# Kernel optimization log

Measured on AMD Instinct MI355X. Metric: run time of the kernel, lower is better.

## Reference

```python
import jax, jax.numpy as jnp
from jax import lax
import numpy as np

N_BITS = 108
N_OUT = 7
# pos_bits[i, j] = bit j (MSB-first) of index i, matching `i >> (6 - j) & 1`
POS_BITS = np.array([[(i >> (6 - j)) & 1 for j in range(N_OUT)] for i in range(N_BITS)], dtype=np.float32)
# LZC value when all 108 bits are zero: 108 = 1101100b, MSB first
LZC_108 = np.array([1, 1, 0, 1, 1, 0, 0], dtype=np.float32)


def setup_inputs() -> dict:
    key = jax.random.key(0)
    # sparse binary bits so leading-zero runs are long and some rows are all-zero
    X = (jax.random.uniform(key, (2_000_000, N_BITS)) < 0.03).astype(jnp.float32)
    return {"X": X}


def _lzd(X):
    """X: [..., 108] MSB-first bits -> [..., 7] LZC MSB-first.

    Arithmetic soft-gate semantics: NOT(a)=1-a, AND(a,b)=a*b,
    OR(a,b)=a+b-a*b, MUX(s,a,b)=s*a+(1-s)*b, OR-tree = 1-prod(1-x).
    Sequential carry over `found` expressed with lax.scan (108 steps).
    """
    batch_shape = X.shape[:-1]
    bits = jnp.moveaxis(X, -1, 0)  # [108, ...]
    pos = jnp.asarray(POS_BITS, dtype=X.dtype)  # [108, 7]

    def step(carry, inp):
        found, lzc = carry                  # found: [..., 1], lzc: [..., 7]
        bit, pos_bits = inp                 # bit: [...], pos_bits: [7]
        bit = bit[..., None]                # [..., 1]
        not_found = 1.0 - found             # NOT
        is_first = bit * not_found          # AND
        # MUX per output bit: is_first ? pos_bit : lzc
        lzc = is_first * pos_bits + (1.0 - is_first) * lzc
        # OR: found | is_first
        found = found + is_first - found * is_first
        return (found, lzc), None

    found0 = jnp.zeros(batch_shape + (1,), X.dtype)
    lzc0 = jnp.zeros(batch_shape + (N_OUT,), X.dtype)
    (found, lzc), _ = lax.scan(step, (found0, lzc0), (bits, pos))

    # OR-tree over all 108 bits, then all-zero override with LZC=108
    any_one = 1.0 - jnp.prod(1.0 - X, axis=-1, keepdims=True)  # [..., 1]
    all_zero = 1.0 - any_one                                   # NOT
    lzc108 = jnp.asarray(LZC_108, dtype=X.dtype)               # [7]
    return all_zero * lzc108 + (1.0 - all_zero) * lzc


def reference(X):
    return _lzd(X)
```

## Files before the change

kernel.cpp:

```cpp
#include <hip/hip_runtime.h>


#define LZD_NBITS 108
#define LZD_NOUT 7
#define RPB 256
#define F4R 27
#define F4B (RPB * F4R)
#define KPAD 28

static __device__ __forceinline__ unsigned umin_(unsigned a, unsigned b) {
    return a < b ? a : b;
}

__global__ __launch_bounds__(256) void lzd108_kernel(const float* __restrict__ X,
                                                     float* __restrict__ out,
                                                     int n_rows) {
    __shared__ unsigned short keys[RPB][KPAD];
    const int tid = threadIdx.x;
    const size_t row0 = (size_t)blockIdx.x * RPB;
    const float4* __restrict__ p =
        reinterpret_cast<const float4*>(X) + row0 * F4R;

    keys[tid][F4R] = (unsigned short)0xFFFFu;

    const size_t nf4_rem = ((size_t)n_rows - row0) * F4R;

    if (nf4_rem >= (size_t)F4B) {
        #pragma unroll
        for (int it = 0; it < F4B / RPB; ++it) {
            const int i = tid + it * RPB;
            const float4 v = p[i];
            const int r = i / F4R;
            const int c = i - r * F4R;
            const unsigned sub = (v.x != 0.0f) ? 0u
                               : (v.y != 0.0f) ? 1u
                               : (v.z != 0.0f) ? 2u
                               : (v.w != 0.0f) ? 3u : 4u;
            keys[r][c] = (sub == 4u) ? (unsigned short)0xFFFFu
                                     : (unsigned short)(4u * (unsigned)c + sub);
        }
    } else {
        const int nf4 = (int)nf4_rem;
        #pragma unroll 1
        for (int i = tid; i < nf4; i += RPB) {
            const float4 v = p[i];
            const int r = i / F4R;
            const int c = i - r * F4R;
            const unsigned sub = (v.x != 0.0f) ? 0u
                               : (v.y != 0.0f) ? 1u
                               : (v.z != 0.0f) ? 2u
                               : (v.w != 0.0f) ? 3u : 4u;
            keys[r][c] = (sub == 4u) ? (unsigned short)0xFFFFu
                                     : (unsigned short)(4u * (unsigned)c + sub);
        }
    }
    __syncthreads();

    const size_t row = row0 + (size_t)tid;
    if (row < (size_t)n_rows) {
        const uint2* kp = reinterpret_cast<const uint2*>(&keys[tid][0]);
        unsigned m = 0xFFFFu;
        #pragma unroll
        for (int j = 0; j < 7; ++j) {
            const uint2 u = kp[j];
            m = umin_(m, umin_(umin_(u.x & 0xFFFFu, u.x >> 16),
                               umin_(u.y & 0xFFFFu, u.y >> 16)));
        }
        const unsigned idx = (m > 107u) ? (unsigned)LZD_NBITS : m;
        float* o = out + row * LZD_NOUT;
        o[0] = (float)((idx >> 6) & 1u);
        o[1] = (float)((idx >> 5) & 1u);
        o[2] = (float)((idx >> 4) & 1u);
        o[3] = (float)((idx >> 3) & 1u);
        o[4] = (float)((idx >> 2) & 1u);
        o[5] = (float)((idx >> 1) & 1u);
        o[6] = (float)(idx & 1u);
    }
}

extern "C" void kernel_launch(void* const* d_in, const int* in_sizes, int n_in,
                              void* d_out, int out_size, void* d_ws, size_t ws_size,
                              hipStream_t stream) {
    const float* X = (const float*)d_in[0];
    float* out = (float*)d_out;
    int n_rows = in_sizes[0] / LZD_NBITS;
    int block = 256;
    int grid = (n_rows + RPB - 1) / RPB;
    lzd108_kernel<<<grid, block, 0, stream>>>(X, out, n_rows);
}
```

Before: 1.116 ms.

## Stage outputs in shared memory for coalesced stores and batch loads in groups

Per-thread output writes, which were strided by 7 floats, are replaced by staging the results in shared memory and then issuing coalesced block-wide stores. Input loads are issued in groups of 9 per iteration instead of a fully unrolled loop, which bounds register pressure while keeping several loads in flight. The zero test now uses integer comparisons instead of float comparisons. The cost is an extra barrier and more shared memory. Integer tests would treat -0.0 as nonzero, which cannot occur with these binary inputs.

```diff
diff --git a/kernel.cpp b/kernel.cpp
--- a/kernel.cpp
+++ b/kernel.cpp
@@ -2,79 +2,98 @@
 
 
 #define LZD_NBITS 108
-#define LZD_NOUT 7
-#define RPB 256
-#define F4R 27
-#define F4B (RPB * F4R)
+#define LZD_NOUT  7
+#define RPB  256
+#define F4R  27
+#define F4B  (RPB * F4R)
 #define KPAD 28
-
-static __device__ __forceinline__ unsigned umin_(unsigned a, unsigned b) {
-    return a < b ? a : b;
-}
+#define GRP  9
 
 __global__ __launch_bounds__(256) void lzd108_kernel(const float* __restrict__ X,
                                                      float* __restrict__ out,
                                                      int n_rows) {
     __shared__ unsigned short keys[RPB][KPAD];
+    __shared__ float outs[RPB * LZD_NOUT];
+
     const int tid = threadIdx.x;
     const size_t row0 = (size_t)blockIdx.x * RPB;
-    const float4* __restrict__ p =
-        reinterpret_cast<const float4*>(X) + row0 * F4R;
+    const uint4* __restrict__ p =
+        reinterpret_cast<const uint4*>(X) + row0 * F4R;
 
     keys[tid][F4R] = (unsigned short)0xFFFFu;
 
     const size_t nf4_rem = ((size_t)n_rows - row0) * F4R;
 
     if (nf4_rem >= (size_t)F4B) {
-        #pragma unroll
-        for (int it = 0; it < F4B / RPB; ++it) {
-            const int i = tid + it * RPB;
-            const float4 v = p[i];
-            const int r = i / F4R;
-            const int c = i - r * F4R;
-            const unsigned sub = (v.x != 0.0f) ? 0u
-                               : (v.y != 0.0f) ? 1u
-                               : (v.z != 0.0f) ? 2u
-                               : (v.w != 0.0f) ? 3u : 4u;
-            keys[r][c] = (sub == 4u) ? (unsigned short)0xFFFFu
-                                     : (unsigned short)(4u * (unsigned)c + sub);
+        #pragma unroll 1
+        for (int g = 0; g < F4R / GRP; ++g) {
+            uint4 v[GRP];
+            #pragma unroll
+            for (int u = 0; u < GRP; ++u)
+                v[u] = p[tid + (g * GRP + u) * RPB];
+            #pragma unroll
+            for (int u = 0; u < GRP; ++u) {
+                const int i = tid + (g * GRP + u) * RPB;
+                const int r = i / F4R;
+                const int c = i - r * F4R;
+                const uint4 w = v[u];
+                const unsigned sub = w.x ? 0u : w.y ? 1u : w.z ? 2u
+                                   : w.w ? 3u : 4u;
+                keys[r][c] = (sub == 4u)
+                                 ? (unsigned short)0xFFFFu
+                                 : (unsigned short)(4u * (unsigned)c + sub);
+            }
         }
     } else {
         const int nf4 = (int)nf4_rem;
         #pragma unroll 1
         for (int i = tid; i < nf4; i += RPB) {
-            const float4 v = p[i];
+            const uint4 w = p[i];
             const int r = i / F4R;
             const int c = i - r * F4R;
-            const unsigned sub = (v.x != 0.0f) ? 0u
-                               : (v.y != 0.0f) ? 1u
-                               : (v.z != 0.0f) ? 2u
-                               : (v.w != 0.0f) ? 3u : 4u;
-            keys[r][c] = (sub == 4u) ? (unsigned short)0xFFFFu
-                                     : (unsigned short)(4u * (unsigned)c + sub);
+            const unsigned sub = w.x ? 0u : w.y ? 1u : w.z ? 2u
+                               : w.w ? 3u : 4u;
+            keys[r][c] = (sub == 4u)
+                             ? (unsigned short)0xFFFFu
+                             : (unsigned short)(4u * (unsigned)c + sub);
         }
     }
     __syncthreads();
 
-    const size_t row = row0 + (size_t)tid;
-    if (row < (size_t)n_rows) {
+    const int nvalid_l = n_rows - (int)row0;
+    const int nvalid = nvalid_l < RPB ? nvalid_l : RPB;
+
+    if (tid < nvalid) {
         const uint2* kp = reinterpret_cast<const uint2*>(&keys[tid][0]);
         unsigned m = 0xFFFFu;
         #pragma unroll
         for (int j = 0; j < 7; ++j) {
             const uint2 u = kp[j];
-            m = umin_(m, umin_(umin_(u.x & 0xFFFFu, u.x >> 16),
-                               umin_(u.y & 0xFFFFu, u.y >> 16)));
+            const unsigned a = u.x & 0xFFFFu, b = u.x >> 16;
+            const unsigned c2 = u.y & 0xFFFFu, d = u.y >> 16;
+            const unsigned ab = a < b ? a : b;
+            const unsigned cd = c2 < d ? c2 : d;
+            const unsigned e = ab < cd ? ab : cd;
+            m = m < e ? m : e;
         }
         const unsigned idx = (m > 107u) ? (unsigned)LZD_NBITS : m;
-        float* o = out + row * LZD_NOUT;
-        o[0] = (float)((idx >> 6) & 1u);
-        o[1] = (float)((idx >> 5) & 1u);
-        o[2] = (float)((idx >> 4) & 1u);
-        o[3] = (float)((idx >> 3) & 1u);
-        o[4] = (float)((idx >> 2) & 1u);
-        o[5] = (float)((idx >> 1) & 1u);
-        o[6] = (float)(idx & 1u);
+        float* os = &outs[tid * LZD_NOUT];
+        os[0] = (float)((idx >> 6) & 1u);
+        os[1] = (float)((idx >> 5) & 1u);
+        os[2] = (float)((idx >> 4) & 1u);
+        os[3] = (float)((idx >> 3) & 1u);
+        os[4] = (float)((idx >> 2) & 1u);
+        os[5] = (float)((idx >> 1) & 1u);
+        os[6] = (float)(idx & 1u);
+    }
+    __syncthreads();
+
+    const int limit = nvalid * LZD_NOUT;
+    float* ob = out + row0 * LZD_NOUT;
+    #pragma unroll
+    for (int j = 0; j < LZD_NOUT; ++j) {
+        const int k = tid + j * RPB;
+        if (k < limit) ob[k] = outs[k];
     }
 }
 
```

Result: faster. 1.088 ms (-2.5%).

## Early-exit per-row scan with bitmask ffs, two rows per thread

Applied to the files above, without the earlier changes.

Replaces the coalesced full-row load plus shared-memory min reduction with a per-thread scan that handles two rows. Each thread loads 16-float chunks, packs their sign/exponent bits into a mask, and stops at the first nonzero chunk, so it can skip reading the rest of the row. Outputs for the two rows are written together as float2 stores. The cost is uncoalesced, divergent per-thread loads, which may lower effective bandwidth. With 3% density, most rows find a set bit within the first one or two chunks, though whole cache lines are still fetched.

```diff
diff --git a/kernel.cpp b/kernel.cpp
--- a/kernel.cpp
+++ b/kernel.cpp
@@ -3,78 +3,93 @@
 
 #define LZD_NBITS 108
 #define LZD_NOUT 7
-#define RPB 256
-#define F4R 27
-#define F4B (RPB * F4R)
-#define KPAD 28
 
-static __device__ __forceinline__ unsigned umin_(unsigned a, unsigned b) {
-    return a < b ? a : b;
-}
+#define MASK16(a, b, c, d)                                              \
+    ( ((a).x >> 23 & 1u)   | ((a).y >> 22 & 2u)   |                     \
+      ((a).z >> 21 & 4u)   | ((a).w >> 20 & 8u)   |                     \
+      ((b).x >> 19 & 16u)  | ((b).y >> 18 & 32u)  |                     \
+      ((b).z >> 17 & 64u)  | ((b).w >> 16 & 128u) |                     \
+      ((c).x >> 15 & 256u) | ((c).y >> 14 & 512u) |                     \
+      ((c).z >> 13 & 1024u)| ((c).w >> 12 & 2048u)|                     \
+      ((d).x >> 11 & 4096u)| ((d).y >> 10 & 8192u)|                     \
+      ((d).z >> 9 & 16384u)| ((d).w >> 8 & 32768u) )
+
+#define ROW_ROUND(P, off, etot, pos, done)                              \
+    if (!(done)) {                                                      \
+        const int e_ = (etot) - 16 * k;                                 \
+        if (k < 7 || e_ > 0) {                                          \
+            uint4 a_, b_, c_, d_;                                       \
+            a_ = (P)[4 * k];                                            \
+            if (k < 6) {                                                \
+                b_ = (P)[4 * k + 1];                                    \
+                c_ = (P)[4 * k + 2];                                    \
+                d_ = (P)[4 * k + 3];                                    \
+            } else if (k == 6) {                                        \
+                b_ = (P)[4 * k + 1];                                    \
+                c_ = (P)[4 * k + 2];                                    \
+                d_ = make_uint4(0u, 0u, 0u, 0u);                        \
+                if (e_ > 12) d_ = (P)[4 * k + 3];                       \
+            } else {                                                    \
+                b_ = make_uint4(0u, 0u, 0u, 0u);                        \
+                c_ = make_uint4(0u, 0u, 0u, 0u);                        \
+                d_ = make_uint4(0u, 0u, 0u, 0u);                        \
+                if (e_ > 4) b_ = (P)[4 * k + 1];                        \
+            }                                                           \
+            unsigned m_ = MASK16(a_, b_, c_, d_);                       \
+            if (k == 0) m_ &= ~((1u << (off)) - 1u);                    \
+            if (k >= 6) { if (e_ < 16) m_ &= (1u << e_) - 1u; }         \
+            if (m_) {                                                   \
+                (pos) = 16 * k + (__ffs(m_) - 1) - (int)(off);          \
+                (done) = true;                                          \
+            } else if (k >= 6 && e_ <= 16) {                            \
+                (done) = true;            \
+            }                                                           \
+        } else {                                                        \
+            (done) = true;                                              \
+        }                                                               \
+    }
 
 __global__ __launch_bounds__(256) void lzd108_kernel(const float* __restrict__ X,
                                                      float* __restrict__ out,
                                                      int n_rows) {
-    __shared__ unsigned short keys[RPB][KPAD];
-    const int tid = threadIdx.x;
-    const size_t row0 = (size_t)blockIdx.x * RPB;
-    const float4* __restrict__ p =
-        reinterpret_cast<const float4*>(X) + row0 * F4R;
+    const int t = blockIdx.x * blockDim.x + threadIdx.x;
+    const int r0 = 2 * t;
+    if (r0 >= n_rows) return;
+    const bool has1 = (r0 + 1) < n_rows;
 
-    keys[tid][F4R] = (unsigned short)0xFFFFu;
+    const unsigned off0 = (unsigned)(((unsigned)r0 * 108u) & 15u);
+    const unsigned off1 = (unsigned)(((unsigned)(r0 + 1) * 108u) & 15u);
+    const uint4* __restrict__ P0 =
+        reinterpret_cast<const uint4*>(X + (size_t)r0 * 108u - off0);
+    const uint4* __restrict__ P1 =
+        reinterpret_cast<const uint4*>(X + (size_t)(r0 + 1) * 108u - off1);
+    const int e0t = (int)off0 + LZD_NBITS;
+    const int e1t = (int)off1 + LZD_NBITS;
 
-    const size_t nf4_rem = ((size_t)n_rows - row0) * F4R;
+    int pos0 = LZD_NBITS, pos1 = LZD_NBITS;
+    bool d0 = false, d1 = !has1;
 
-    if (nf4_rem >= (size_t)F4B) {
+    #pragma unroll
+    for (int k = 0; k < 8; ++k) {
+        if (d0 && d1) break;
+        ROW_ROUND(P0, off0, e0t, pos0, d0)
+        ROW_ROUND(P1, off1, e1t, pos1, d1)
+    }
+
+    float* o = out + (size_t)r0 * LZD_NOUT;
+    if (has1) {
+        float v[14];
         #pragma unroll
-        for (int it = 0; it < F4B / RPB; ++it) {
-            const int i = tid + it * RPB;
-            const float4 v = p[i];
-            const int r = i / F4R;
-            const int c = i - r * F4R;
-            const unsigned sub = (v.x != 0.0f) ? 0u
-                               : (v.y != 0.0f) ? 1u
-                               : (v.z != 0.0f) ? 2u
-                               : (v.w != 0.0f) ? 3u : 4u;
-            keys[r][c] = (sub == 4u) ? (unsigned short)0xFFFFu
-                                     : (unsigned short)(4u * (unsigned)c + sub);
-        }
+        for (int j = 0; j < 7; ++j) v[j] = (float)((pos0 >> (6 - j)) & 1);
+        #pragma unroll
+        for (int j = 0; j < 7; ++j) v[7 + j] = (float)((pos1 >> (6 - j)) & 1);
+        float2* o2 = reinterpret_cast<float2*>(o);
+        #pragma unroll
+        for (int j = 0; j < 7; ++j)
+            o2[j] = make_float2(v[2 * j], v[2 * j + 1]);
     } else {
-        const int nf4 = (int)nf4_rem;
-        #pragma unroll 1
-        for (int i = tid; i < nf4; i += RPB) {
-            const float4 v = p[i];
-            const int r = i / F4R;
-            const int c = i - r * F4R;
-            const unsigned sub = (v.x != 0.0f) ? 0u
-                               : (v.y != 0.0f) ? 1u
-                               : (v.z != 0.0f) ? 2u
-                               : (v.w != 0.0f) ? 3u : 4u;
-            keys[r][c] = (sub == 4u) ? (unsigned short)0xFFFFu
-                                     : (unsigned short)(4u * (unsigned)c + sub);
-        }
-    }
-    __syncthreads();
-
-    const size_t row = row0 + (size_t)tid;
-    if (row < (size_t)n_rows) {
-        const uint2* kp = reinterpret_cast<const uint2*>(&keys[tid][0]);
-        unsigned m = 0xFFFFu;
         #pragma unroll
-        for (int j = 0; j < 7; ++j) {
-            const uint2 u = kp[j];
-            m = umin_(m, umin_(umin_(u.x & 0xFFFFu, u.x >> 16),
-                               umin_(u.y & 0xFFFFu, u.y >> 16)));
-        }
-        const unsigned idx = (m > 107u) ? (unsigned)LZD_NBITS : m;
-        float* o = out + row * LZD_NOUT;
-        o[0] = (float)((idx >> 6) & 1u);
-        o[1] = (float)((idx >> 5) & 1u);
-        o[2] = (float)((idx >> 4) & 1u);
-        o[3] = (float)((idx >> 3) & 1u);
-        o[4] = (float)((idx >> 2) & 1u);
-        o[5] = (float)((idx >> 1) & 1u);
-        o[6] = (float)(idx & 1u);
+        for (int j = 0; j < 7; ++j) o[j] = (float)((pos0 >> (6 - j)) & 1);
     }
 }
 
@@ -85,6 +100,7 @@
     float* out = (float*)d_out;
     int n_rows = in_sizes[0] / LZD_NBITS;
     int block = 256;
-    int grid = (n_rows + RPB - 1) / RPB;
+    int rows_per_block = 2 * block;
+    int grid = (n_rows + rows_per_block - 1) / rows_per_block;
     lzd108_kernel<<<grid, block, 0, stream>>>(X, out, n_rows);
 }
```

New measurement: 1.029 ms. -7.8%, faster.
